# Kernel optimization log

Measured on AMD Instinct MI355X. Metric: run time of the kernel, lower is better.

The kernel has to match this reference:

```python
import jax, jax.numpy as jnp
import numpy as np

jax.config.update('jax_enable_x64', True)

RES = 0.1
HASH_SIZE = 2 ** 20
D = 120
HEADS = 8
HEAD_DIM = D // HEADS  # 15
MOD_T = 201
BMIN = np.array([-2.6, -8.1, 0.0], dtype=np.float32)
BMAX = np.array([4.6, 4.7, 3.1], dtype=np.float32)
PRIMES = np.array([73856093, 19349669, 83492791], dtype=np.int64)
M = 200000


def _build_buffer():
    axes = [np.arange(BMIN[i], BMAX[i], RES, dtype=np.float32) for i in range(3)]
    g = np.meshgrid(*axes, indexing='ij')
    coords = np.stack(g, axis=-1).reshape(-1, 3)
    n = coords.shape[0]
    grid = np.floor(coords / RES).astype(np.int64)
    h = np.remainder((grid * PRIMES).sum(-1), HASH_SIZE)
    buf = np.full(HASH_SIZE, n, dtype=np.int64)
    # loop assigns in increasing i and keeps the first => min index per hash slot
    np.minimum.at(buf, h, np.arange(n, dtype=np.int64))
    buf = np.where(buf == n, -1, buf)
    return buf, n


def setup_inputs() -> dict:
    key = jax.random.key(0)
    ks = jax.random.split(key, 9)
    buf, n_vox = _build_buffer()
    pts = jnp.asarray(BMIN) + jax.random.uniform(ks[0], (M, 3), dtype=jnp.float32) * jnp.asarray(BMAX - BMIN)
    times = jax.random.randint(ks[1], (M,), 0, 1000, dtype=jnp.int64)
    scale = float(1.0 / np.sqrt(D))
    return {
        'query_pts': pts,
        'query_times': times,
        'buffer_voxel_index': jnp.asarray(buf),
        'static_features': 0.01 * jax.random.normal(ks[2], (n_vox, D), dtype=jnp.float32),
        'dynamic_features': 0.01 * jax.random.normal(ks[3], (n_vox, D), dtype=jnp.float32),
        'time_embeddings': 0.01 * jax.random.normal(ks[4], (MOD_T, D), dtype=jnp.float32),
        'fusion_td_w': scale * jax.random.normal(ks[5], (4, D, D), dtype=jnp.float32),
        'fusion_td_b': jnp.zeros((4, D), dtype=jnp.float32),
        'fusion_sd_w': scale * jax.random.normal(ks[6], (4, D, D), dtype=jnp.float32),
        'fusion_sd_b': jnp.zeros((4, D), dtype=jnp.float32),
    }


def _fusion(a, b, W, B):
    # LocalSelfAttentionFusion: 2-token multi-head self-attention over [a; b],
    # returning the attended first token. W/B stack (q, k, v, out) projections.
    m = a.shape[0]
    tok = jnp.stack([a, b], axis=1)  # [M, 2, D]
    q = (tok @ W[0] + B[0]).reshape(m, 2, HEADS, HEAD_DIM)
    k = (tok @ W[1] + B[1]).reshape(m, 2, HEADS, HEAD_DIM)
    v = (tok @ W[2] + B[2]).reshape(m, 2, HEADS, HEAD_DIM)
    s = jnp.einsum('mqhd,mkhd->mhqk', q, k) * np.float32(1.0 / np.sqrt(HEAD_DIM))
    p = jax.nn.softmax(s, axis=-1)  # [M, H, 2, 2]
    o = jnp.einsum('mhqk,mkhd->mqhd', p, v).reshape(m, 2, D)
    return (o @ W[3] + B[3])[:, 0]  # fused token, [M, D]


def reference(query_pts, query_times, buffer_voxel_index, static_features, dynamic_features,
              time_embeddings, fusion_td_w, fusion_td_b, fusion_sd_w, fusion_sd_b):
    grid = jnp.floor(query_pts / RES).astype(jnp.int64)
    h = jnp.remainder((grid * jnp.asarray(PRIMES)).sum(-1), HASH_SIZE)
    v_idx = buffer_voxel_index[h]              # [M]
    valid = v_idx >= 0
    vi = jnp.where(valid, v_idx, 0)            # safe gather index
    ti = jnp.remainder(query_times, MOD_T)
    sf = static_features[vi]                   # [M, D]
    df = dynamic_features[vi]                  # [M, D]
    te = time_embeddings[ti]                   # [M, D]
    cond = _fusion(df, te, fusion_td_w, fusion_td_b)
    fused = _fusion(sf, cond, fusion_sd_w, fusion_sd_b)
    return jnp.where(valid[:, None], fused, jnp.float32(0))
```

## Files before the change

### kernel.cpp

```cpp
#include <hip/hip_runtime.h>
#include <math.h>

#define DD   120
#define KPAD 128
#define KP   136
#define MT   64
#define NTHR 512
#define HASH_MASK 1048575LL
#define MODT 201

typedef short  short8  __attribute__((ext_vector_type(8)));
typedef float  floatx4 __attribute__((ext_vector_type(4)));

__device__ __forceinline__ unsigned short f2b(float f) {
    __bf16 h = (__bf16)f;
    return __builtin_bit_cast(unsigned short, h);
}
__device__ __forceinline__ float b2f(unsigned short u) {
    unsigned int x = ((unsigned int)u) << 16;
    return __builtin_bit_cast(float, x);
}
__device__ __forceinline__ float rsum16(float v) {
    v += __shfl_xor(v, 1, 16);
    v += __shfl_xor(v, 2, 16);
    v += __shfl_xor(v, 4, 16);
    v += __shfl_xor(v, 8, 16);
    return v;
}
__device__ __forceinline__ uint2 pack4(float4 v) {
    unsigned int lo = (unsigned int)f2b(v.x) | ((unsigned int)f2b(v.y) << 16);
    unsigned int hi = (unsigned int)f2b(v.z) | ((unsigned int)f2b(v.w) << 16);
    return make_uint2(lo, hi);
}

__global__ __launch_bounds__(256)
void prep_weights(const float* __restrict__ td_w, const float* __restrict__ sd_w,
                  unsigned short* __restrict__ wt)
{
    int idx = blockIdx.x * 256 + threadIdx.x;
    int mat = idx >> 14;
    int k   = (idx >> 7) & 127;
    int n   = idx & 127;
    const float* src = (mat < 4) ? (td_w + mat * DD * DD) : (sd_w + (mat - 4) * DD * DD);
    float v = (n < DD && k < DD) ? src[k * DD + n] : 0.f;
    wt[(mat << 14) + (n << 7) + k] = f2b(v);
}

__global__ __launch_bounds__(128)
void prep_te(const float* __restrict__ temb, const float* __restrict__ td_w,
             const float* __restrict__ td_b,
             unsigned short* __restrict__ k1t, unsigned short* __restrict__ v1t)
{
    int t = blockIdx.x;
    int n = threadIdx.x;
    float a1 = 0.f, a2 = 0.f;
    if (n < DD) {
        a1 = td_b[DD + n];
        a2 = td_b[2 * DD + n];
        const float* te = temb + t * DD;
        const float* w1 = td_w + 1 * DD * DD;
        const float* w2 = td_w + 2 * DD * DD;
        for (int k = 0; k < DD; k++) {
            float x = te[k];
            a1 = fmaf(x, w1[k * DD + n], a1);
            a2 = fmaf(x, w2[k * DD + n], a2);
        }
    }
    k1t[t * KPAD + n] = f2b(a1);
    v1t[t * KPAD + n] = f2b(a2);
}

__device__ __forceinline__ void gemm_tile(const unsigned short* IN,
                                          const unsigned short* __restrict__ WT,
                                          const float* __restrict__ bias,
                                          unsigned short* OUT,
                                          int lm, int lq, int n0)
{
    const int n = n0 + lm;
    short8 bfr[4];
#pragma unroll
    for (int ks = 0; ks < 4; ks++)
        bfr[ks] = *(const short8*)(WT + n * KPAD + ks * 32 + lq * 8);
    float bv = (n < DD) ? bias[n] : 0.f;
#pragma unroll
    for (int mt = 0; mt < 4; mt++) {
        floatx4 acc = {0.f, 0.f, 0.f, 0.f};
#pragma unroll
        for (int ks = 0; ks < 4; ks++) {
            short8 a = *(const short8*)(IN + (mt * 16 + lm) * KP + ks * 32 + lq * 8);
            acc = __builtin_amdgcn_mfma_f32_16x16x32_bf16(a, bfr[ks], acc, 0, 0, 0);
        }
#pragma unroll
        for (int r = 0; r < 4; r++)
            OUT[(mt * 16 + lq * 4 + r) * KP + n] = f2b(acc[r] + bv);
    }
}

__device__ __forceinline__ void gemm_out(const unsigned short* IN,
                                         const unsigned short* __restrict__ WT,
                                         const float* __restrict__ bias,
                                         float* __restrict__ out,
                                         const int* s_valid, int pbase, int Mpts,
                                         int lm, int lq, int n0)
{
    const int n = n0 + lm;
    short8 bfr[4];
#pragma unroll
    for (int ks = 0; ks < 4; ks++)
        bfr[ks] = *(const short8*)(WT + n * KPAD + ks * 32 + lq * 8);
    float bv = (n < DD) ? bias[n] : 0.f;
#pragma unroll
    for (int mt = 0; mt < 4; mt++) {
        floatx4 acc = {0.f, 0.f, 0.f, 0.f};
#pragma unroll
        for (int ks = 0; ks < 4; ks++) {
            short8 a = *(const short8*)(IN + (mt * 16 + lm) * KP + ks * 32 + lq * 8);
            acc = __builtin_amdgcn_mfma_f32_16x16x32_bf16(a, bfr[ks], acc, 0, 0, 0);
        }
        if (n < DD) {
#pragma unroll
            for (int r = 0; r < 4; r++) {
                int row = mt * 16 + lq * 4 + r;
                int gp = pbase + row;
                if (gp < Mpts)
                    out[(size_t)gp * DD + n] = s_valid[row] ? (acc[r] + bv) : 0.f;
            }
        }
    }
}

__global__ __launch_bounds__(NTHR, 4)
void voxel_mfma_kernel(const float* __restrict__ pts,
                       const int* __restrict__ times,
                       const int* __restrict__ vox_buf,
                       const float* __restrict__ stat_f,
                       const float* __restrict__ dyn_f,
                       const float* __restrict__ td_b,
                       const float* __restrict__ sd_b,
                       const unsigned short* __restrict__ wt,
                       const unsigned short* __restrict__ k1t,
                       const unsigned short* __restrict__ v1t,
                       float* __restrict__ out,
                       int Mpts)
{
    __shared__ __align__(16) unsigned short sA[MT * KP];
    __shared__ __align__(16) unsigned short sC[MT * KP];
    __shared__ __align__(16) unsigned short sO[MT * KP];
    __shared__ int s_vi[MT];
    __shared__ int s_valid[MT];
    __shared__ int s_ti[MT];

    const int tid  = threadIdx.x;
    const int lane = tid & 63;
    const int lm   = lane & 15;
    const int lq   = lane >> 4;
    const int wv   = tid >> 6;
    const int n0h  = wv * 15;
    const int n0t  = wv * 16;
    const int nn   = n0h + lm;
    const int pbase = blockIdx.x * MT;
    const float scale = 0.2581988897471611f;
    const float msk = (lm < 15) ? 1.f : 0.f;

    short8 bq[4], bk[4], bvv[4];
    {
        const unsigned short* w0 = wt + 0 * 16384;
        const unsigned short* w1 = wt + 1 * 16384;
        const unsigned short* w2 = wt + 2 * 16384;
#pragma unroll
        for (int ks = 0; ks < 4; ks++) {
            bq[ks]  = *(const short8*)(w0 + nn * KPAD + ks * 32 + lq * 8);
            bk[ks]  = *(const short8*)(w1 + nn * KPAD + ks * 32 + lq * 8);
            bvv[ks] = *(const short8*)(w2 + nn * KPAD + ks * 32 + lq * 8);
        }
    }
    const float f1bq = td_b[nn];
    const float f1bk = td_b[120 + nn];
    const float f1bv = td_b[240 + nn];

    if (tid < MT) {
        int p = pbase + tid;
        int vi = 0, valid = 0, ti = 0;
        if (p < Mpts) {
            float x = pts[3 * p + 0];
            float y = pts[3 * p + 1];
            float z = pts[3 * p + 2];
            long long gx = (long long)floorf(x / 0.1f);
            long long gy = (long long)floorf(y / 0.1f);
            long long gz = (long long)floorf(z / 0.1f);
            long long hh = (gx * 73856093LL + gy * 19349669LL + gz * 83492791LL) & HASH_MASK;
            int v = vox_buf[(int)hh];
            valid = (v >= 0) ? 1 : 0;
            vi = (v >= 0) ? v : 0;
            ti = times[p] % MODT;
        }
        s_vi[tid] = vi; s_valid[tid] = valid; s_ti[tid] = ti;
    }
    if (tid < 256) {
        int b = tid >> 7, p = (tid >> 1) & 63, q = tid & 1;
        unsigned short* B = b ? sO : sA;
        *(uint2*)(B + p * KP + 120 + q * 4) = make_uint2(0u, 0u);
    }
    __syncthreads();

    for (int i = tid; i < MT * 30; i += NTHR) {
        int p = i / 30, f = i % 30;
        float4 v = *(const float4*)(dyn_f + (size_t)s_vi[p] * DD + f * 4);
        *(uint2*)(sA + p * KP + f * 4) = pack4(v);
    }
    __syncthreads();

#pragma unroll
    for (int mt = 0; mt < 4; mt++) {
        short8 a[4];
#pragma unroll
        for (int ks = 0; ks < 4; ks++)
            a[ks] = *(const short8*)(sA + (mt * 16 + lm) * KP + ks * 32 + lq * 8);
        int4 tiv = *(const int4*)(s_ti + mt * 16 + lq * 4);
        int tt[4] = {tiv.x, tiv.y, tiv.z, tiv.w};
        float k1v[4], v1v[4];
#pragma unroll
        for (int r = 0; r < 4; r++) {
            k1v[r] = b2f(k1t[tt[r] * KPAD + nn]);
            v1v[r] = b2f(v1t[tt[r] * KPAD + nn]);
        }
        floatx4 q = {0.f,0.f,0.f,0.f}, k0 = {0.f,0.f,0.f,0.f}, v0 = {0.f,0.f,0.f,0.f};
#pragma unroll
        for (int ks = 0; ks < 4; ks++) {
            q  = __builtin_amdgcn_mfma_f32_16x16x32_bf16(a[ks], bq[ks],  q,  0, 0, 0);
            k0 = __builtin_amdgcn_mfma_f32_16x16x32_bf16(a[ks], bk[ks],  k0, 0, 0, 0);
            v0 = __builtin_amdgcn_mfma_f32_16x16x32_bf16(a[ks], bvv[ks], v0, 0, 0, 0);
        }
#pragma unroll
        for (int r = 0; r < 4; r++) {
            float qf = (q[r] + f1bq) * msk;
            float c0 = rsum16(qf * (k0[r] + f1bk));
            float c1 = rsum16(qf * k1v[r]);
            float p0 = 1.f / (1.f + expf((c1 - c0) * scale));
            float o  = p0 * (v0[r] + f1bv) + (1.f - p0) * v1v[r];
            if (lm < 15)
                sO[(mt * 16 + lq * 4 + r) * KP + nn] = f2b(o);
        }
    }
    __syncthreads();

    {
        float4 g0, g1, g2, g3 = {0.f,0.f,0.f,0.f};
        int a0, a1, a2, a3 = -1;
        {
            int i = tid, p = i / 30, f = i % 30;
            g0 = *(const float4*)(stat_f + (size_t)s_vi[p] * DD + f * 4);
            a0 = p * KP + f * 4;
            i += NTHR; p = i / 30; f = i % 30;
            g1 = *(const float4*)(stat_f + (size_t)s_vi[p] * DD + f * 4);
            a1 = p * KP + f * 4;
            i += NTHR; p = i / 30; f = i % 30;
            g2 = *(const float4*)(stat_f + (size_t)s_vi[p] * DD + f * 4);
            a2 = p * KP + f * 4;
            i += NTHR;
            if (i < MT * 30) {
                p = i / 30; f = i % 30;
                g3 = *(const float4*)(stat_f + (size_t)s_vi[p] * DD + f * 4);
                a3 = p * KP + f * 4;
            }
        }
        gemm_tile(sO, wt + 3 * 16384, td_b + 360, sC, lm, lq, n0t);
        *(uint2*)(sA + a0) = pack4(g0);
        *(uint2*)(sA + a1) = pack4(g1);
        *(uint2*)(sA + a2) = pack4(g2);
        if (a3 >= 0) *(uint2*)(sA + a3) = pack4(g3);
    }
    __syncthreads();

    {
        const unsigned short* u0 = wt + 4 * 16384;
        const unsigned short* u1 = wt + 5 * 16384;
        const unsigned short* u2 = wt + 6 * 16384;
        short8 c1f[4], c2f[4];
#pragma unroll
        for (int ks = 0; ks < 4; ks++) {
            c1f[ks] = *(const short8*)(u1 + nn * KPAD + ks * 32 + lq * 8);
            c2f[ks] = *(const short8*)(u2 + nn * KPAD + ks * 32 + lq * 8);
        }
        const float f2bq = sd_b[nn];
        const float f2bk = sd_b[120 + nn];
        const float f2bv = sd_b[240 + nn];
#pragma unroll
        for (int mt = 0; mt < 4; mt++) {
            short8 a[4], c[4];
#pragma unroll
            for (int ks = 0; ks < 4; ks++) {
                a[ks] = *(const short8*)(sA + (mt * 16 + lm) * KP + ks * 32 + lq * 8);
                c[ks] = *(const short8*)(sC + (mt * 16 + lm) * KP + ks * 32 + lq * 8);
            }
            floatx4 q = {0.f,0.f,0.f,0.f}, k20 = {0.f,0.f,0.f,0.f}, k21 = {0.f,0.f,0.f,0.f};
#pragma unroll
            for (int ks = 0; ks < 4; ks++) {
                short8 b0 = *(const short8*)(u0 + nn * KPAD + ks * 32 + lq * 8);
                q   = __builtin_amdgcn_mfma_f32_16x16x32_bf16(a[ks], b0,      q,   0, 0, 0);
                k20 = __builtin_amdgcn_mfma_f32_16x16x32_bf16(a[ks], c1f[ks], k20, 0, 0, 0);
                k21 = __builtin_amdgcn_mfma_f32_16x16x32_bf16(c[ks], c1f[ks], k21, 0, 0, 0);
            }
            float p0a[4];
#pragma unroll
            for (int r = 0; r < 4; r++) {
                float qf = (q[r] + f2bq) * msk;
                float c0 = rsum16(qf * (k20[r] + f2bk));
                float c1 = rsum16(qf * (k21[r] + f2bk));
                p0a[r] = 1.f / (1.f + expf((c1 - c0) * scale));
            }
            floatx4 v20 = {0.f,0.f,0.f,0.f}, v21 = {0.f,0.f,0.f,0.f};
#pragma unroll
            for (int ks = 0; ks < 4; ks++) {
                v20 = __builtin_amdgcn_mfma_f32_16x16x32_bf16(a[ks], c2f[ks], v20, 0, 0, 0);
                v21 = __builtin_amdgcn_mfma_f32_16x16x32_bf16(c[ks], c2f[ks], v21, 0, 0, 0);
            }
#pragma unroll
            for (int r = 0; r < 4; r++) {
                float o = p0a[r] * (v20[r] + f2bv) + (1.f - p0a[r]) * (v21[r] + f2bv);
                if (lm < 15)
                    sO[(mt * 16 + lq * 4 + r) * KP + nn] = f2b(o);
            }
        }
    }
    __syncthreads();

    gemm_out(sO, wt + 7 * 16384, sd_b + 360, out, s_valid, pbase, Mpts, lm, lq, n0t);
}

extern "C" void kernel_launch(void* const* d_in, const int* in_sizes, int n_in,
                              void* d_out, int out_size, void* d_ws, size_t ws_size,
                              hipStream_t stream) {
    const float* pts   = (const float*)d_in[0];
    const int*   times = (const int*)d_in[1];
    const int*   vox   = (const int*)d_in[2];
    const float* statf = (const float*)d_in[3];
    const float* dynf  = (const float*)d_in[4];
    const float* temb  = (const float*)d_in[5];
    const float* td_w  = (const float*)d_in[6];
    const float* td_b  = (const float*)d_in[7];
    const float* sd_w  = (const float*)d_in[8];
    const float* sd_b  = (const float*)d_in[9];

    unsigned short* wt  = (unsigned short*)d_ws;
    unsigned short* k1t = wt + 8 * 128 * 128;
    unsigned short* v1t = k1t + 201 * 128;

    prep_weights<<<512, 256, 0, stream>>>(td_w, sd_w, wt);
    prep_te<<<201, 128, 0, stream>>>(temb, td_w, td_b, k1t, v1t);

    int Mpts = in_sizes[0] / 3;
    int blocks = (Mpts + MT - 1) / MT;
    voxel_mfma_kernel<<<blocks, NTHR, 0, stream>>>(
        pts, times, vox, statf, dynf, td_b, sd_b, wt, k1t, v1t,
        (float*)d_out, Mpts);
}
```

Before: 483.0 us.

## Make voxel kernel persistent with software-pipelined prefetch of next tile's gathers

Turns the per-tile kernel into a persistent grid-stride loop capped at 768 blocks, with double-buffered per-point index arrays in shared memory. The next tile's point coordinates, hash lookup and dynamic-feature gather are issued during the current tile's compute stages, so global-memory latency is hidden behind the MFMA work. The cost is fewer resident blocks when there are fewer tiles than slots, and weight fragments are reloaded every iteration. A fixed grid cap may also underfill or unbalance the device.

```diff
diff --git a/kernel.cpp b/kernel.cpp
--- a/kernel.cpp
+++ b/kernel.cpp
@@ -8,6 +8,7 @@
 #define NTHR 512
 #define HASH_MASK 1048575LL
 #define MODT 201
+#define MAXGRID 768
 
 typedef short  short8  __attribute__((ext_vector_type(8)));
 typedef float  floatx4 __attribute__((ext_vector_type(4)));
@@ -146,9 +147,9 @@
     __shared__ __align__(16) unsigned short sA[MT * KP];
     __shared__ __align__(16) unsigned short sC[MT * KP];
     __shared__ __align__(16) unsigned short sO[MT * KP];
-    __shared__ int s_vi[MT];
-    __shared__ int s_valid[MT];
-    __shared__ int s_ti[MT];
+    __shared__ __align__(16) int s_vi[2][MT];
+    __shared__ __align__(16) int s_valid[2][MT];
+    __shared__ __align__(16) int s_ti[2][MT];
 
     const int tid  = threadIdx.x;
     const int lane = tid & 63;
@@ -158,28 +159,26 @@
     const int n0h  = wv * 15;
     const int n0t  = wv * 16;
     const int nn   = n0h + lm;
-    const int pbase = blockIdx.x * MT;
     const float scale = 0.2581988897471611f;
     const float msk = (lm < 15) ? 1.f : 0.f;
-
-    short8 bq[4], bk[4], bvv[4];
-    {
-        const unsigned short* w0 = wt + 0 * 16384;
-        const unsigned short* w1 = wt + 1 * 16384;
-        const unsigned short* w2 = wt + 2 * 16384;
-#pragma unroll
-        for (int ks = 0; ks < 4; ks++) {
-            bq[ks]  = *(const short8*)(w0 + nn * KPAD + ks * 32 + lq * 8);
-            bk[ks]  = *(const short8*)(w1 + nn * KPAD + ks * 32 + lq * 8);
-            bvv[ks] = *(const short8*)(w2 + nn * KPAD + ks * 32 + lq * 8);
-        }
-    }
+    const int ntiles = (Mpts + MT - 1) / MT;
+
+    if ((int)blockIdx.x >= ntiles) return;
+
     const float f1bq = td_b[nn];
     const float f1bk = td_b[120 + nn];
     const float f1bv = td_b[240 + nn];
-
+    const float f2bq = sd_b[nn];
+    const float f2bk = sd_b[120 + nn];
+    const float f2bv = sd_b[240 + nn];
+
+    if (tid < 256) {
+        int b = tid >> 7, p = (tid >> 1) & 63, q = tid & 1;
+        unsigned short* B = b ? sO : sA;
+        *(uint2*)(B + p * KP + 120 + q * 4) = make_uint2(0u, 0u);
+    }
     if (tid < MT) {
-        int p = pbase + tid;
+        int p = blockIdx.x * MT + tid;
         int vi = 0, valid = 0, ti = 0;
         if (p < Mpts) {
             float x = pts[3 * p + 0];
@@ -194,138 +193,206 @@
             vi = (v >= 0) ? v : 0;
             ti = times[p] % MODT;
         }
-        s_vi[tid] = vi; s_valid[tid] = valid; s_ti[tid] = ti;
-    }
-    if (tid < 256) {
-        int b = tid >> 7, p = (tid >> 1) & 63, q = tid & 1;
-        unsigned short* B = b ? sO : sA;
-        *(uint2*)(B + p * KP + 120 + q * 4) = make_uint2(0u, 0u);
+        s_vi[0][tid] = vi; s_valid[0][tid] = valid; s_ti[0][tid] = ti;
     }
     __syncthreads();
-
     for (int i = tid; i < MT * 30; i += NTHR) {
         int p = i / 30, f = i % 30;
-        float4 v = *(const float4*)(dyn_f + (size_t)s_vi[p] * DD + f * 4);
+        float4 v = *(const float4*)(dyn_f + (size_t)s_vi[0][p] * DD + f * 4);
         *(uint2*)(sA + p * KP + f * 4) = pack4(v);
     }
     __syncthreads();
 
-#pragma unroll
-    for (int mt = 0; mt < 4; mt++) {
-        short8 a[4];
-#pragma unroll
-        for (int ks = 0; ks < 4; ks++)
-            a[ks] = *(const short8*)(sA + (mt * 16 + lm) * KP + ks * 32 + lq * 8);
-        int4 tiv = *(const int4*)(s_ti + mt * 16 + lq * 4);
-        int tt[4] = {tiv.x, tiv.y, tiv.z, tiv.w};
-        float k1v[4], v1v[4];
-#pragma unroll
-        for (int r = 0; r < 4; r++) {
-            k1v[r] = b2f(k1t[tt[r] * KPAD + nn]);
-            v1v[r] = b2f(v1t[tt[r] * KPAD + nn]);
-        }
-        floatx4 q = {0.f,0.f,0.f,0.f}, k0 = {0.f,0.f,0.f,0.f}, v0 = {0.f,0.f,0.f,0.f};
-#pragma unroll
-        for (int ks = 0; ks < 4; ks++) {
-            q  = __builtin_amdgcn_mfma_f32_16x16x32_bf16(a[ks], bq[ks],  q,  0, 0, 0);
-            k0 = __builtin_amdgcn_mfma_f32_16x16x32_bf16(a[ks], bk[ks],  k0, 0, 0, 0);
-            v0 = __builtin_amdgcn_mfma_f32_16x16x32_bf16(a[ks], bvv[ks], v0, 0, 0, 0);
-        }
-#pragma unroll
-        for (int r = 0; r < 4; r++) {
-            float qf = (q[r] + f1bq) * msk;
-            float c0 = rsum16(qf * (k0[r] + f1bk));
-            float c1 = rsum16(qf * k1v[r]);
-            float p0 = 1.f / (1.f + expf((c1 - c0) * scale));
-            float o  = p0 * (v0[r] + f1bv) + (1.f - p0) * v1v[r];
-            if (lm < 15)
-                sO[(mt * 16 + lq * 4 + r) * KP + nn] = f2b(o);
-        }
-    }
-    __syncthreads();
-
-    {
-        float4 g0, g1, g2, g3 = {0.f,0.f,0.f,0.f};
-        int a0, a1, a2, a3 = -1;
+    int cur = 0;
+    for (int tile = blockIdx.x; tile < ntiles; tile += gridDim.x) {
+        const int pbase   = tile * MT;
+        const int nxtile  = tile + gridDim.x;
+        const bool hasnext = (nxtile < ntiles);
+        const int nxt = cur ^ 1;
+
+        float npx = 0.f, npy = 0.f, npz = 0.f; int ntim = 0;
+        if (hasnext && tid < MT) {
+            int p = nxtile * MT + tid;
+            if (p < Mpts) {
+                npx = pts[3 * p + 0];
+                npy = pts[3 * p + 1];
+                npz = pts[3 * p + 2];
+                ntim = times[p];
+            }
+        }
         {
-            int i = tid, p = i / 30, f = i % 30;
-            g0 = *(const float4*)(stat_f + (size_t)s_vi[p] * DD + f * 4);
-            a0 = p * KP + f * 4;
-            i += NTHR; p = i / 30; f = i % 30;
-            g1 = *(const float4*)(stat_f + (size_t)s_vi[p] * DD + f * 4);
-            a1 = p * KP + f * 4;
-            i += NTHR; p = i / 30; f = i % 30;
-            g2 = *(const float4*)(stat_f + (size_t)s_vi[p] * DD + f * 4);
-            a2 = p * KP + f * 4;
-            i += NTHR;
-            if (i < MT * 30) {
-                p = i / 30; f = i % 30;
-                g3 = *(const float4*)(stat_f + (size_t)s_vi[p] * DD + f * 4);
-                a3 = p * KP + f * 4;
-            }
-        }
-        gemm_tile(sO, wt + 3 * 16384, td_b + 360, sC, lm, lq, n0t);
-        *(uint2*)(sA + a0) = pack4(g0);
-        *(uint2*)(sA + a1) = pack4(g1);
-        *(uint2*)(sA + a2) = pack4(g2);
-        if (a3 >= 0) *(uint2*)(sA + a3) = pack4(g3);
-    }
-    __syncthreads();
-
-    {
-        const unsigned short* u0 = wt + 4 * 16384;
-        const unsigned short* u1 = wt + 5 * 16384;
-        const unsigned short* u2 = wt + 6 * 16384;
-        short8 c1f[4], c2f[4];
-#pragma unroll
-        for (int ks = 0; ks < 4; ks++) {
-            c1f[ks] = *(const short8*)(u1 + nn * KPAD + ks * 32 + lq * 8);
-            c2f[ks] = *(const short8*)(u2 + nn * KPAD + ks * 32 + lq * 8);
-        }
-        const float f2bq = sd_b[nn];
-        const float f2bk = sd_b[120 + nn];
-        const float f2bv = sd_b[240 + nn];
-#pragma unroll
-        for (int mt = 0; mt < 4; mt++) {
-            short8 a[4], c[4];
+            const unsigned short* w0 = wt + 0 * 16384;
+            const unsigned short* w1 = wt + 1 * 16384;
+            const unsigned short* w2 = wt + 2 * 16384;
+            short8 bq[4], bk[4], bvv[4];
 #pragma unroll
             for (int ks = 0; ks < 4; ks++) {
-                a[ks] = *(const short8*)(sA + (mt * 16 + lm) * KP + ks * 32 + lq * 8);
-                c[ks] = *(const short8*)(sC + (mt * 16 + lm) * KP + ks * 32 + lq * 8);
-            }
-            floatx4 q = {0.f,0.f,0.f,0.f}, k20 = {0.f,0.f,0.f,0.f}, k21 = {0.f,0.f,0.f,0.f};
+                bq[ks]  = *(const short8*)(w0 + nn * KPAD + ks * 32 + lq * 8);
+                bk[ks]  = *(const short8*)(w1 + nn * KPAD + ks * 32 + lq * 8);
+                bvv[ks] = *(const short8*)(w2 + nn * KPAD + ks * 32 + lq * 8);
+            }
+#pragma unroll
+            for (int mt = 0; mt < 4; mt++) {
+                short8 a[4];
+#pragma unroll
+                for (int ks = 0; ks < 4; ks++)
+                    a[ks] = *(const short8*)(sA + (mt * 16 + lm) * KP + ks * 32 + lq * 8);
+                int4 tiv = *(const int4*)(&s_ti[cur][mt * 16 + lq * 4]);
+                int tt[4] = {tiv.x, tiv.y, tiv.z, tiv.w};
+                float k1v[4], v1v[4];
+#pragma unroll
+                for (int r = 0; r < 4; r++) {
+                    k1v[r] = b2f(k1t[tt[r] * KPAD + nn]);
+                    v1v[r] = b2f(v1t[tt[r] * KPAD + nn]);
+                }
+                floatx4 q = {0.f,0.f,0.f,0.f}, k0 = {0.f,0.f,0.f,0.f}, v0 = {0.f,0.f,0.f,0.f};
+#pragma unroll
+                for (int ks = 0; ks < 4; ks++) {
+                    q  = __builtin_amdgcn_mfma_f32_16x16x32_bf16(a[ks], bq[ks],  q,  0, 0, 0);
+                    k0 = __builtin_amdgcn_mfma_f32_16x16x32_bf16(a[ks], bk[ks],  k0, 0, 0, 0);
+                    v0 = __builtin_amdgcn_mfma_f32_16x16x32_bf16(a[ks], bvv[ks], v0, 0, 0, 0);
+                }
+#pragma unroll
+                for (int r = 0; r < 4; r++) {
+                    float qf = (q[r] + f1bq) * msk;
+                    float c0 = rsum16(qf * (k0[r] + f1bk));
+                    float c1 = rsum16(qf * k1v[r]);
+                    float p0 = 1.f / (1.f + expf((c1 - c0) * scale));
+                    float o  = p0 * (v0[r] + f1bv) + (1.f - p0) * v1v[r];
+                    if (lm < 15)
+                        sO[(mt * 16 + lq * 4 + r) * KP + nn] = f2b(o);
+                }
+            }
+        }
+        __syncthreads();
+
+        int nv = -1;
+        if (hasnext && tid < MT) {
+            int p = nxtile * MT + tid;
+            if (p < Mpts) {
+                long long gx = (long long)floorf(npx / 0.1f);
+                long long gy = (long long)floorf(npy / 0.1f);
+                long long gz = (long long)floorf(npz / 0.1f);
+                long long hh = (gx * 73856093LL + gy * 19349669LL + gz * 83492791LL) & HASH_MASK;
+                nv = vox_buf[(int)hh];
+            }
+        }
+        {
+            float4 g0, g1, g2, g3 = {0.f,0.f,0.f,0.f};
+            int a0, a1, a2, a3 = -1;
+            {
+                int i = tid, p = i / 30, f = i % 30;
+                g0 = *(const float4*)(stat_f + (size_t)s_vi[cur][p] * DD + f * 4);
+                a0 = p * KP + f * 4;
+                i += NTHR; p = i / 30; f = i % 30;
+                g1 = *(const float4*)(stat_f + (size_t)s_vi[cur][p] * DD + f * 4);
+                a1 = p * KP + f * 4;
+                i += NTHR; p = i / 30; f = i % 30;
+                g2 = *(const float4*)(stat_f + (size_t)s_vi[cur][p] * DD + f * 4);
+                a2 = p * KP + f * 4;
+                i += NTHR;
+                if (i < MT * 30) {
+                    p = i / 30; f = i % 30;
+                    g3 = *(const float4*)(stat_f + (size_t)s_vi[cur][p] * DD + f * 4);
+                    a3 = p * KP + f * 4;
+                }
+            }
+            gemm_tile(sO, wt + 3 * 16384, td_b + 360, sC, lm, lq, n0t);
+            *(uint2*)(sA + a0) = pack4(g0);
+            *(uint2*)(sA + a1) = pack4(g1);
+            *(uint2*)(sA + a2) = pack4(g2);
+            if (a3 >= 0) *(uint2*)(sA + a3) = pack4(g3);
+        }
+        __syncthreads();
+
+        if (hasnext && tid < MT) {
+            s_vi[nxt][tid]    = (nv >= 0) ? nv : 0;
+            s_valid[nxt][tid] = (nv >= 0) ? 1 : 0;
+            s_ti[nxt][tid]    = ntim % MODT;
+        }
+        {
+            const unsigned short* u0 = wt + 4 * 16384;
+            const unsigned short* u1 = wt + 5 * 16384;
+            const unsigned short* u2 = wt + 6 * 16384;
+            short8 c1f[4], c2f[4];
 #pragma unroll
             for (int ks = 0; ks < 4; ks++) {
-                short8 b0 = *(const short8*)(u0 + nn * KPAD + ks * 32 + lq * 8);
-                q   = __builtin_amdgcn_mfma_f32_16x16x32_bf16(a[ks], b0,      q,   0, 0, 0);
-                k20 = __builtin_amdgcn_mfma_f32_16x16x32_bf16(a[ks], c1f[ks], k20, 0, 0, 0);
-                k21 = __builtin_amdgcn_mfma_f32_16x16x32_bf16(c[ks], c1f[ks], k21, 0, 0, 0);
-            }
-            float p0a[4];
-#pragma unroll
-            for (int r = 0; r < 4; r++) {
-                float qf = (q[r] + f2bq) * msk;
-                float c0 = rsum16(qf * (k20[r] + f2bk));
-                float c1 = rsum16(qf * (k21[r] + f2bk));
-                p0a[r] = 1.f / (1.f + expf((c1 - c0) * scale));
-            }
-            floatx4 v20 = {0.f,0.f,0.f,0.f}, v21 = {0.f,0.f,0.f,0.f};
-#pragma unroll
-            for (int ks = 0; ks < 4; ks++) {
-                v20 = __builtin_amdgcn_mfma_f32_16x16x32_bf16(a[ks], c2f[ks], v20, 0, 0, 0);
-                v21 = __builtin_amdgcn_mfma_f32_16x16x32_bf16(c[ks], c2f[ks], v21, 0, 0, 0);
-            }
-#pragma unroll
-            for (int r = 0; r < 4; r++) {
-                float o = p0a[r] * (v20[r] + f2bv) + (1.f - p0a[r]) * (v21[r] + f2bv);
-                if (lm < 15)
-                    sO[(mt * 16 + lq * 4 + r) * KP + nn] = f2b(o);
-            }
-        }
-    }
-    __syncthreads();
-
-    gemm_out(sO, wt + 7 * 16384, sd_b + 360, out, s_valid, pbase, Mpts, lm, lq, n0t);
+                c1f[ks] = *(const short8*)(u1 + nn * KPAD + ks * 32 + lq * 8);
+                c2f[ks] = *(const short8*)(u2 + nn * KPAD + ks * 32 + lq * 8);
+            }
+#pragma unroll
+            for (int mt = 0; mt < 4; mt++) {
+                short8 a[4], c[4];
+#pragma unroll
+                for (int ks = 0; ks < 4; ks++) {
+                    a[ks] = *(const short8*)(sA + (mt * 16 + lm) * KP + ks * 32 + lq * 8);
+                    c[ks] = *(const short8*)(sC + (mt * 16 + lm) * KP + ks * 32 + lq * 8);
+                }
+                floatx4 q = {0.f,0.f,0.f,0.f}, k20 = {0.f,0.f,0.f,0.f}, k21 = {0.f,0.f,0.f,0.f};
+#pragma unroll
+                for (int ks = 0; ks < 4; ks++) {
+                    short8 b0 = *(const short8*)(u0 + nn * KPAD + ks * 32 + lq * 8);
+                    q   = __builtin_amdgcn_mfma_f32_16x16x32_bf16(a[ks], b0,      q,   0, 0, 0);
+                    k20 = __builtin_amdgcn_mfma_f32_16x16x32_bf16(a[ks], c1f[ks], k20, 0, 0, 0);
+                    k21 = __builtin_amdgcn_mfma_f32_16x16x32_bf16(c[ks], c1f[ks], k21, 0, 0, 0);
+                }
+                float p0a[4];
+#pragma unroll
+                for (int r = 0; r < 4; r++) {
+                    float qf = (q[r] + f2bq) * msk;
+                    float c0 = rsum16(qf * (k20[r] + f2bk));
+                    float c1 = rsum16(qf * (k21[r] + f2bk));
+                    p0a[r] = 1.f / (1.f + expf((c1 - c0) * scale));
+                }
+                floatx4 v20 = {0.f,0.f,0.f,0.f}, v21 = {0.f,0.f,0.f,0.f};
+#pragma unroll
+                for (int ks = 0; ks < 4; ks++) {
+                    v20 = __builtin_amdgcn_mfma_f32_16x16x32_bf16(a[ks], c2f[ks], v20, 0, 0, 0);
+                    v21 = __builtin_amdgcn_mfma_f32_16x16x32_bf16(c[ks], c2f[ks], v21, 0, 0, 0);
+                }
+#pragma unroll
+                for (int r = 0; r < 4; r++) {
+                    float o = p0a[r] * (v20[r] + f2bv) + (1.f - p0a[r]) * (v21[r] + f2bv);
+                    if (lm < 15)
+                        sO[(mt * 16 + lq * 4 + r) * KP + nn] = f2b(o);
+                }
+            }
+        }
+        __syncthreads();
+
+        if (hasnext) {
+            float4 g0, g1, g2, g3 = {0.f,0.f,0.f,0.f};
+            int a0, a1, a2, a3 = -1;
+            {
+                int i = tid, p = i / 30, f = i % 30;
+                g0 = *(const float4*)(dyn_f + (size_t)s_vi[nxt][p] * DD + f * 4);
+                a0 = p * KP + f * 4;
+                i += NTHR; p = i / 30; f = i % 30;
+                g1 = *(const float4*)(dyn_f + (size_t)s_vi[nxt][p] * DD + f * 4);
+                a1 = p * KP + f * 4;
+                i += NTHR; p = i / 30; f = i % 30;
+                g2 = *(const float4*)(dyn_f + (size_t)s_vi[nxt][p] * DD + f * 4);
+                a2 = p * KP + f * 4;
+                i += NTHR;
+                if (i < MT * 30) {
+                    p = i / 30; f = i % 30;
+                    g3 = *(const float4*)(dyn_f + (size_t)s_vi[nxt][p] * DD + f * 4);
+                    a3 = p * KP + f * 4;
+                }
+            }
+            gemm_out(sO, wt + 7 * 16384, sd_b + 360, out, &s_valid[cur][0],
+                     pbase, Mpts, lm, lq, n0t);
+            *(uint2*)(sA + a0) = pack4(g0);
+            *(uint2*)(sA + a1) = pack4(g1);
+            *(uint2*)(sA + a2) = pack4(g2);
+            if (a3 >= 0) *(uint2*)(sA + a3) = pack4(g3);
+        } else {
+            gemm_out(sO, wt + 7 * 16384, sd_b + 360, out, &s_valid[cur][0],
+                     pbase, Mpts, lm, lq, n0t);
+        }
+        __syncthreads();
+        cur = nxt;
+    }
 }
 
 extern "C" void kernel_launch(void* const* d_in, const int* in_sizes, int n_in,
@@ -350,7 +417,8 @@
     prep_te<<<201, 128, 0, stream>>>(temb, td_w, td_b, k1t, v1t);
 
     int Mpts = in_sizes[0] / 3;
-    int blocks = (Mpts + MT - 1) / MT;
+    int ntiles = (Mpts + MT - 1) / MT;
+    int blocks = (ntiles < MAXGRID) ? ntiles : MAXGRID;
     voxel_mfma_kernel<<<blocks, NTHR, 0, stream>>>(
         pts, times, vox, statf, dynf, td_b, sd_b, wt, k1t, v1t,
         (float*)d_out, Mpts);
```

After: 702.6 us. 45.5% more time.

## Halve point tile to 32 with 256 threads, DPP reductions and exp2/rcp softmax

Applied to the files above, without the earlier changes.

Shrinks each block from 64 points and 8 waves to 32 points and 4 waves, so each wave now covers two heads and two output column tiles. Weight fragments are reloaded per head instead of being held in registers across the kernel, and launch bounds are raised to allow more resident blocks. The 16-lane reductions use DPP row-shift adds instead of shuffles, and the 2-way softmax uses exp2 with a prescaled constant and a hardware reciprocal. This trades more weight reloads and blocks for better occupancy, cheaper reductions and a slightly less accurate softmax.

```diff
diff --git a/kernel.cpp b/kernel.cpp
--- a/kernel.cpp
+++ b/kernel.cpp
@@ -4,8 +4,9 @@
 #define DD   120
 #define KPAD 128
 #define KP   136
-#define MT   64
-#define NTHR 512
+#define MT   32
+#define MTB  2
+#define NTHR 256
 #define HASH_MASK 1048575LL
 #define MODT 201
 
@@ -20,11 +21,17 @@
     unsigned int x = ((unsigned int)u) << 16;
     return __builtin_bit_cast(float, x);
 }
+template<int CTRL>
+__device__ __forceinline__ float dpp_add(float v) {
+    int y = __builtin_amdgcn_update_dpp(0, __builtin_bit_cast(int, v),
+                                        CTRL, 0xF, 0xF, false);
+    return v + __builtin_bit_cast(float, y);
+}
 __device__ __forceinline__ float rsum16(float v) {
-    v += __shfl_xor(v, 1, 16);
-    v += __shfl_xor(v, 2, 16);
-    v += __shfl_xor(v, 4, 16);
-    v += __shfl_xor(v, 8, 16);
+    v = dpp_add<0x128>(v);
+    v = dpp_add<0x124>(v);
+    v = dpp_add<0x122>(v);
+    v = dpp_add<0x121>(v);
     return v;
 }
 __device__ __forceinline__ uint2 pack4(float4 v) {
@@ -83,7 +90,7 @@
         bfr[ks] = *(const short8*)(WT + n * KPAD + ks * 32 + lq * 8);
     float bv = (n < DD) ? bias[n] : 0.f;
 #pragma unroll
-    for (int mt = 0; mt < 4; mt++) {
+    for (int mt = 0; mt < MTB; mt++) {
         floatx4 acc = {0.f, 0.f, 0.f, 0.f};
 #pragma unroll
         for (int ks = 0; ks < 4; ks++) {
@@ -110,7 +117,7 @@
         bfr[ks] = *(const short8*)(WT + n * KPAD + ks * 32 + lq * 8);
     float bv = (n < DD) ? bias[n] : 0.f;
 #pragma unroll
-    for (int mt = 0; mt < 4; mt++) {
+    for (int mt = 0; mt < MTB; mt++) {
         floatx4 acc = {0.f, 0.f, 0.f, 0.f};
 #pragma unroll
         for (int ks = 0; ks < 4; ks++) {
@@ -129,7 +136,7 @@
     }
 }
 
-__global__ __launch_bounds__(NTHR, 4)
+__global__ __launch_bounds__(NTHR, 6)
 void voxel_mfma_kernel(const float* __restrict__ pts,
                        const int* __restrict__ times,
                        const int* __restrict__ vox_buf,
@@ -146,37 +153,18 @@
     __shared__ __align__(16) unsigned short sA[MT * KP];
     __shared__ __align__(16) unsigned short sC[MT * KP];
     __shared__ __align__(16) unsigned short sO[MT * KP];
-    __shared__ int s_vi[MT];
-    __shared__ int s_valid[MT];
-    __shared__ int s_ti[MT];
+    __shared__ __align__(16) int s_vi[MT];
+    __shared__ __align__(16) int s_valid[MT];
+    __shared__ __align__(16) int s_ti[MT];
 
     const int tid  = threadIdx.x;
     const int lane = tid & 63;
     const int lm   = lane & 15;
     const int lq   = lane >> 4;
     const int wv   = tid >> 6;
-    const int n0h  = wv * 15;
-    const int n0t  = wv * 16;
-    const int nn   = n0h + lm;
     const int pbase = blockIdx.x * MT;
-    const float scale = 0.2581988897471611f;
+    const float kscale = 0.37250226f;
     const float msk = (lm < 15) ? 1.f : 0.f;
-
-    short8 bq[4], bk[4], bvv[4];
-    {
-        const unsigned short* w0 = wt + 0 * 16384;
-        const unsigned short* w1 = wt + 1 * 16384;
-        const unsigned short* w2 = wt + 2 * 16384;
-#pragma unroll
-        for (int ks = 0; ks < 4; ks++) {
-            bq[ks]  = *(const short8*)(w0 + nn * KPAD + ks * 32 + lq * 8);
-            bk[ks]  = *(const short8*)(w1 + nn * KPAD + ks * 32 + lq * 8);
-            bvv[ks] = *(const short8*)(w2 + nn * KPAD + ks * 32 + lq * 8);
-        }
-    }
-    const float f1bq = td_b[nn];
-    const float f1bk = td_b[120 + nn];
-    const float f1bv = td_b[240 + nn];
 
     if (tid < MT) {
         int p = pbase + tid;
@@ -196,10 +184,10 @@
         }
         s_vi[tid] = vi; s_valid[tid] = valid; s_ti[tid] = ti;
     }
-    if (tid < 256) {
-        int b = tid >> 7, p = (tid >> 1) & 63, q = tid & 1;
+    if (tid < 64) {
+        int b = tid >> 5, p = tid & 31;
         unsigned short* B = b ? sO : sA;
-        *(uint2*)(B + p * KP + 120 + q * 4) = make_uint2(0u, 0u);
+        *(uint4*)(B + p * KP + 120) = make_uint4(0u, 0u, 0u, 0u);
     }
     __syncthreads();
 
@@ -211,35 +199,53 @@
     __syncthreads();
 
 #pragma unroll
-    for (int mt = 0; mt < 4; mt++) {
-        short8 a[4];
-#pragma unroll
-        for (int ks = 0; ks < 4; ks++)
-            a[ks] = *(const short8*)(sA + (mt * 16 + lm) * KP + ks * 32 + lq * 8);
-        int4 tiv = *(const int4*)(s_ti + mt * 16 + lq * 4);
-        int tt[4] = {tiv.x, tiv.y, tiv.z, tiv.w};
-        float k1v[4], v1v[4];
-#pragma unroll
-        for (int r = 0; r < 4; r++) {
-            k1v[r] = b2f(k1t[tt[r] * KPAD + nn]);
-            v1v[r] = b2f(v1t[tt[r] * KPAD + nn]);
-        }
-        floatx4 q = {0.f,0.f,0.f,0.f}, k0 = {0.f,0.f,0.f,0.f}, v0 = {0.f,0.f,0.f,0.f};
+    for (int hh = 0; hh < 2; hh++) {
+        const int nn = (2 * wv + hh) * 15 + lm;
+        const unsigned short* w0 = wt + 0 * 16384;
+        const unsigned short* w1 = wt + 1 * 16384;
+        const unsigned short* w2 = wt + 2 * 16384;
+        short8 bq[4], bk[4], bvv[4];
 #pragma unroll
         for (int ks = 0; ks < 4; ks++) {
-            q  = __builtin_amdgcn_mfma_f32_16x16x32_bf16(a[ks], bq[ks],  q,  0, 0, 0);
-            k0 = __builtin_amdgcn_mfma_f32_16x16x32_bf16(a[ks], bk[ks],  k0, 0, 0, 0);
-            v0 = __builtin_amdgcn_mfma_f32_16x16x32_bf16(a[ks], bvv[ks], v0, 0, 0, 0);
-        }
-#pragma unroll
-        for (int r = 0; r < 4; r++) {
-            float qf = (q[r] + f1bq) * msk;
-            float c0 = rsum16(qf * (k0[r] + f1bk));
-            float c1 = rsum16(qf * k1v[r]);
-            float p0 = 1.f / (1.f + expf((c1 - c0) * scale));
-            float o  = p0 * (v0[r] + f1bv) + (1.f - p0) * v1v[r];
-            if (lm < 15)
-                sO[(mt * 16 + lq * 4 + r) * KP + nn] = f2b(o);
+            bq[ks]  = *(const short8*)(w0 + nn * KPAD + ks * 32 + lq * 8);
+            bk[ks]  = *(const short8*)(w1 + nn * KPAD + ks * 32 + lq * 8);
+            bvv[ks] = *(const short8*)(w2 + nn * KPAD + ks * 32 + lq * 8);
+        }
+        const float f1bq = td_b[nn];
+        const float f1bk = td_b[120 + nn];
+        const float f1bv = td_b[240 + nn];
+#pragma unroll
+        for (int mt = 0; mt < MTB; mt++) {
+            short8 a[4];
+#pragma unroll
+            for (int ks = 0; ks < 4; ks++)
+                a[ks] = *(const short8*)(sA + (mt * 16 + lm) * KP + ks * 32 + lq * 8);
+            int4 tiv = *(const int4*)(&s_ti[mt * 16 + lq * 4]);
+            int tt[4] = {tiv.x, tiv.y, tiv.z, tiv.w};
+            float k1v[4], v1v[4];
+#pragma unroll
+            for (int r = 0; r < 4; r++) {
+                k1v[r] = b2f(k1t[tt[r] * KPAD + nn]);
+                v1v[r] = b2f(v1t[tt[r] * KPAD + nn]);
+            }
+            floatx4 q = {0.f,0.f,0.f,0.f}, k0 = {0.f,0.f,0.f,0.f}, v0 = {0.f,0.f,0.f,0.f};
+#pragma unroll
+            for (int ks = 0; ks < 4; ks++) {
+                q  = __builtin_amdgcn_mfma_f32_16x16x32_bf16(a[ks], bq[ks],  q,  0, 0, 0);
+                k0 = __builtin_amdgcn_mfma_f32_16x16x32_bf16(a[ks], bk[ks],  k0, 0, 0, 0);
+                v0 = __builtin_amdgcn_mfma_f32_16x16x32_bf16(a[ks], bvv[ks], v0, 0, 0, 0);
+            }
+#pragma unroll
+            for (int r = 0; r < 4; r++) {
+                float qf = (q[r] + f1bq) * msk;
+                float c0 = rsum16(qf * (k0[r] + f1bk));
+                float c1 = rsum16(qf * k1v[r]);
+                float e  = exp2f((c1 - c0) * kscale);
+                float p0 = __builtin_amdgcn_rcpf(1.f + e);
+                float o  = p0 * (v0[r] + f1bv) + (e * p0) * v1v[r];
+                if (lm < 15)
+                    sO[(mt * 16 + lq * 4 + r) * KP + nn] = f2b(o);
+            }
         }
     }
     __syncthreads();
@@ -264,7 +270,8 @@
                 a3 = p * KP + f * 4;
             }
         }
-        gemm_tile(sO, wt + 3 * 16384, td_b + 360, sC, lm, lq, n0t);
+        gemm_tile(sO, wt + 3 * 16384, td_b + 360, sC, lm, lq, wv * 16);
+        gemm_tile(sO, wt + 3 * 16384, td_b + 360, sC, lm, lq, 64 + wv * 16);
         *(uint2*)(sA + a0) = pack4(g0);
         *(uint2*)(sA + a1) = pack4(g1);
         *(uint2*)(sA + a2) = pack4(g2);
@@ -272,7 +279,9 @@
     }
     __syncthreads();
 
-    {
+#pragma unroll
+    for (int hh = 0; hh < 2; hh++) {
+        const int nn = (2 * wv + hh) * 15 + lm;
         const unsigned short* u0 = wt + 4 * 16384;
         const unsigned short* u1 = wt + 5 * 16384;
         const unsigned short* u2 = wt + 6 * 16384;
@@ -286,7 +295,7 @@
         const float f2bk = sd_b[120 + nn];
         const float f2bv = sd_b[240 + nn];
 #pragma unroll
-        for (int mt = 0; mt < 4; mt++) {
+        for (int mt = 0; mt < MTB; mt++) {
             short8 a[4], c[4];
 #pragma unroll
             for (int ks = 0; ks < 4; ks++) {
@@ -301,13 +310,15 @@
                 k20 = __builtin_amdgcn_mfma_f32_16x16x32_bf16(a[ks], c1f[ks], k20, 0, 0, 0);
                 k21 = __builtin_amdgcn_mfma_f32_16x16x32_bf16(c[ks], c1f[ks], k21, 0, 0, 0);
             }
-            float p0a[4];
+            float p0a[4], p1a[4];
 #pragma unroll
             for (int r = 0; r < 4; r++) {
                 float qf = (q[r] + f2bq) * msk;
                 float c0 = rsum16(qf * (k20[r] + f2bk));
                 float c1 = rsum16(qf * (k21[r] + f2bk));
-                p0a[r] = 1.f / (1.f + expf((c1 - c0) * scale));
+                float e  = exp2f((c1 - c0) * kscale);
+                p0a[r] = __builtin_amdgcn_rcpf(1.f + e);
+                p1a[r] = e * p0a[r];
             }
             floatx4 v20 = {0.f,0.f,0.f,0.f}, v21 = {0.f,0.f,0.f,0.f};
 #pragma unroll
@@ -317,7 +328,7 @@
             }
 #pragma unroll
             for (int r = 0; r < 4; r++) {
-                float o = p0a[r] * (v20[r] + f2bv) + (1.f - p0a[r]) * (v21[r] + f2bv);
+                float o = p0a[r] * (v20[r] + f2bv) + p1a[r] * (v21[r] + f2bv);
                 if (lm < 15)
                     sO[(mt * 16 + lq * 4 + r) * KP + nn] = f2b(o);
             }
@@ -325,7 +336,8 @@
     }
     __syncthreads();
 
-    gemm_out(sO, wt + 7 * 16384, sd_b + 360, out, s_valid, pbase, Mpts, lm, lq, n0t);
+    gemm_out(sO, wt + 7 * 16384, sd_b + 360, out, s_valid, pbase, Mpts, lm, lq, wv * 16);
+    gemm_out(sO, wt + 7 * 16384, sd_b + 360, out, s_valid, pbase, Mpts, lm, lq, 64 + wv * 16);
 }
 
 extern "C" void kernel_launch(void* const* d_in, const int* in_sizes, int n_in,
```

Result: slower. 624.5 us (+29.3%).
